# Performance work log

Hardware: AMD Instinct MI355X
Metric: run time of the kernel (lower is better)

## Reference

```python
import jax, jax.numpy as jnp
import numpy as np

HEADS = 8
EPS = 1e-5
CONV_DIMS = [(16, 32), (32, 64), (64, 128), (128, 256), (256, 128), (128, 128)]


def _bn(x, g, b):
    # BatchNorm over the node dimension (training-mode batch statistics)
    m = x.mean(0)
    v = x.var(0)
    return (x - m) * jax.lax.rsqrt(v + EPS) * g + b


def _feast(x, src, dst, W, U, c, bias, n):
    # FeaStConv: q_h = softmax_h(u_h.(x_j - x_i) + c_h); out_i = mean_j sum_h q_h * (W_h x_j) + bias
    q = jax.nn.softmax((x[src] - x[dst]) @ U + c, axis=-1)          # [E, H]
    f = (x[src] @ W).reshape(src.shape[0], HEADS, -1)               # [E, H, C_out]
    msg = jnp.einsum('ehc,eh->ec', f, q)                            # [E, C_out]
    agg = jax.ops.segment_sum(msg, dst, num_segments=n)
    cnt = jax.ops.segment_sum(jnp.ones_like(dst, dtype=msg.dtype), dst, num_segments=n)
    return agg / cnt[:, None] + bias


def reference(pos, x, g0, b0, lin0_W, lin0_b,
              W0, U0, C0, B0, gc0, bc0,
              W1, U1, C1, B1, gc1, bc1,
              W2, U2, C2, B2, gc2, bc2,
              W3, U3, C3, B3, gc3, bc3,
              W4, U4, C4, B4, gc4, bc4,
              W5, U5, C5, B5, gc5, bc5,
              lin1_W, lin1_b, lin2_W, lin2_b, edge_index):
    n = pos.shape[0]
    loops = jnp.arange(n, dtype=edge_index.dtype)                   # PyG FeaStConv adds self-loops
    src = jnp.concatenate([edge_index[0], loops])
    dst = jnp.concatenate([edge_index[1], loops])

    h = _bn(pos, g0, b0)
    h = jnp.concatenate([h, x], axis=1)
    h = jax.nn.relu(h @ lin0_W + lin0_b)

    convs = [(W0, U0, C0, B0, gc0, bc0), (W1, U1, C1, B1, gc1, bc1),
             (W2, U2, C2, B2, gc2, bc2), (W3, U3, C3, B3, gc3, bc3),
             (W4, U4, C4, B4, gc4, bc4), (W5, U5, C5, B5, gc5, bc5)]
    for W, U, c, bias, g, b in convs:
        h = _feast(h, src, dst, W, U, c, bias, n)
        h = jax.nn.relu(_bn(h, g, b))

    h = jax.nn.relu(h @ lin1_W + lin1_b)
    return h @ lin2_W + lin2_b


def setup_inputs() -> dict:
    key = jax.random.key(0)
    N, E = 10000, 160000
    ks = iter(jax.random.split(key, 64))
    d = {}
    d['pos'] = jax.random.normal(next(ks), (N, 2), jnp.float32)
    d['x'] = jax.random.normal(next(ks), (N, 2), jnp.float32)
    d['edge_index'] = jax.random.randint(next(ks), (2, E), 0, N, dtype=jnp.int32)

    def lin(k, i, o):
        return jax.random.normal(k, (i, o), jnp.float32) * np.float32(1.0 / np.sqrt(i))

    d['g0'] = jnp.ones(2, jnp.float32); d['b0'] = jnp.zeros(2, jnp.float32)
    d['lin0_W'] = lin(next(ks), 4, 16); d['lin0_b'] = jnp.zeros(16, jnp.float32)
    for i, (ci, co) in enumerate(CONV_DIMS):
        d[f'W{i}'] = lin(next(ks), ci, HEADS * co)
        d[f'U{i}'] = lin(next(ks), ci, HEADS)
        d[f'C{i}'] = jnp.zeros(HEADS, jnp.float32)
        d[f'B{i}'] = jnp.zeros(co, jnp.float32)
        d[f'gc{i}'] = jnp.ones(co, jnp.float32)
        d[f'bc{i}'] = jnp.zeros(co, jnp.float32)
    d['lin1_W'] = lin(next(ks), 128, 64); d['lin1_b'] = jnp.zeros(64, jnp.float32)
    d['lin2_W'] = lin(next(ks), 64, 2); d['lin2_b'] = jnp.zeros(2, jnp.float32)
    return d
```

## Files before the change

kernel.cpp:

```cpp
#include <hip/hip_runtime.h>
#include <hip/hip_bf16.h>
#include <math.h>

#define HEADS 8
#define EPS 1e-5f

typedef __attribute__((ext_vector_type(8))) _Float16 half8;
typedef __attribute__((ext_vector_type(4))) _Float16 half4;
typedef __attribute__((ext_vector_type(2))) _Float16 half2v;
typedef __attribute__((ext_vector_type(4))) float f32x4;

__device__ __forceinline__ unsigned short f2h(float f) {
    union { _Float16 h; unsigned short u; } v;
    v.h = (_Float16)f;
    return v.u;
}

#define PACK_TOTAL 745472
#define PACK_BLOCKS 2912

__global__ void k_setup1(const float* __restrict__ W0, const float* __restrict__ W1,
                         const float* __restrict__ W2, const float* __restrict__ W3,
                         const float* __restrict__ W4, const float* __restrict__ W5,
                         unsigned short* __restrict__ Bp,
                         const int* __restrict__ ei, int* __restrict__ deg,
                         const float* __restrict__ pos, float* __restrict__ pstats,
                         int E, int N, int degBlocks) {
    int b = blockIdx.x, tid = threadIdx.x;
    if (b < PACK_BLOCKS) {
        int idx = b * 256 + tid;
        const int CI[6]  = {16, 32, 64, 128, 256, 128};
        const int CO[6]  = {32, 64, 128, 256, 128, 128};
        const int COP[6] = {64, 64, 128, 256, 128, 128};
        const int OFF[7] = {0, 8192, 24576, 90112, 352256, 614400, 745472};
        int L = 0;
        while (idx >= OFF[L + 1]) ++L;
        const float* W = L == 0 ? W0 : L == 1 ? W1 : L == 2 ? W2 : L == 3 ? W3 : L == 4 ? W4 : W5;
        int rel = idx - OFF[L];
        int j = rel & 7;
        int lane = (rel >> 3) & 63;
        int t = rel >> 9;
        int nT = COP[L] >> 4;
        int nt = t % nT, kt = t / nT;
        int kk = kt * 32 + ((lane >> 4) << 3) + j;
        int c  = (nt << 4) + (lane & 15);
        int ci = CI[L], co = CO[L];
        float v = 0.f;
        if (c < co) {
            int h = kk / ci, ko = kk % ci;
            v = W[ko * (HEADS * co) + h * co + c];
        }
        Bp[idx] = f2h(v);
    } else if (b < PACK_BLOCKS + degBlocks) {
        int e = (b - PACK_BLOCKS) * 256 + tid;
        int E2 = E + N;
        if (e < E2) {
            int dst = (e < E) ? ei[E + e] : (e - E);
            atomicAdd(&deg[dst], 1);
        }
    } else {
        int gid = (b - PACK_BLOCKS - degBlocks) * 256 + tid;
        int stride = 64 * 256;
        float s0 = 0, s1 = 0, q0 = 0, q1 = 0;
        for (int i = gid; i < N; i += stride) {
            float a = pos[i * 2], bb = pos[i * 2 + 1];
            s0 += a; s1 += bb; q0 += a * a; q1 += bb * bb;
        }
        __shared__ float red[256][4];
        red[tid][0] = s0; red[tid][1] = s1; red[tid][2] = q0; red[tid][3] = q1;
        __syncthreads();
        for (int off = 128; off > 0; off >>= 1) {
            if (tid < off) {
                red[tid][0] += red[tid + off][0]; red[tid][1] += red[tid + off][1];
                red[tid][2] += red[tid + off][2]; red[tid][3] += red[tid + off][3];
            }
            __syncthreads();
        }
        if (tid == 0) {
            atomicAdd(&pstats[0], red[0][0]); atomicAdd(&pstats[1], red[0][1]);
            atomicAdd(&pstats[2], red[0][2]); atomicAdd(&pstats[3], red[0][3]);
        }
    }
}

__global__ void k_scan(const int* __restrict__ deg, int* __restrict__ row_ptr, int n) {
    __shared__ int part[1024];
    int t = threadIdx.x;
    int chunk = (n + 1023) >> 10;
    int begin = t * chunk;
    int end = begin + chunk;
    if (begin > n) begin = n;
    if (end > n) end = n;
    int s = 0;
    for (int i = begin; i < end; ++i) s += deg[i];
    part[t] = s;
    __syncthreads();
    for (int off = 1; off < 1024; off <<= 1) {
        int v = (t >= off) ? part[t - off] : 0;
        __syncthreads();
        part[t] += v;
        __syncthreads();
    }
    int run = (t == 0) ? 0 : part[t - 1];
    for (int i = begin; i < end; ++i) { row_ptr[i] = run; run += deg[i]; }
    if (t == 1023) row_ptr[n] = part[1023];
}

__global__ void k_setup2(const int* __restrict__ ei, const int* __restrict__ row_ptr,
                         int* __restrict__ fill, int* __restrict__ src_sorted,
                         const float* __restrict__ pos, const float* __restrict__ x,
                         const float* __restrict__ pstats, const float* __restrict__ g0,
                         const float* __restrict__ b0, const float* __restrict__ W,
                         const float* __restrict__ bias, const float* __restrict__ U0,
                         _Float16* __restrict__ out, float* __restrict__ xu0,
                         int E, int N, int fillBlocks) {
    int b = blockIdx.x, tid = threadIdx.x;
    if (b < fillBlocks) {
        int e = b * 256 + tid;
        int E2 = E + N;
        if (e < E2) {
            int srcv, dst;
            if (e < E) { srcv = ei[e]; dst = ei[E + e]; } else { srcv = e - E; dst = srcv; }
            int p = atomicAdd(&fill[dst], 1);
            src_sorted[row_ptr[dst] + p] = srcv;
        }
    } else {
        int i = (b - fillBlocks) * 256 + tid;
        if (i >= N) return;
        float invn = 1.0f / (float)N;
        float in4[4];
        #pragma unroll
        for (int j = 0; j < 2; ++j) {
            float m = pstats[j] * invn;
            float v = pstats[2 + j] * invn - m * m;
            in4[j] = (pos[i * 2 + j] - m) * rsqrtf(v + EPS) * g0[j] + b0[j];
        }
        in4[2] = x[i * 2]; in4[3] = x[i * 2 + 1];
        float o16[16];
        #pragma unroll
        for (int o = 0; o < 16; ++o) {
            float s = bias[o];
            #pragma unroll
            for (int j = 0; j < 4; ++j) s += in4[j] * W[j * 16 + o];
            o16[o] = fmaxf(s, 0.f);
            out[i * 16 + o] = (_Float16)o16[o];
        }
        #pragma unroll
        for (int hh = 0; hh < 8; ++hh) {
            float p = 0.f;
            #pragma unroll
            for (int k = 0; k < 16; ++k) p += o16[k] * U0[k * 8 + hh];
            xu0[i * 8 + hh] = p;
        }
    }
}

__device__ __forceinline__ void chunk_softmax(const float* __restrict__ xu,
        const int* __restrict__ srcs, int base, int cnt, int lane,
        float4 xi0, float4 xi1, float4 c0, float4 c1, float dinv,
        float* __restrict__ qrow, int* __restrict__ srow) {
    if (lane < cnt) {
        int s = srcs[base + lane];
        float4 xs0 = *(const float4*)(xu + (size_t)s * 8);
        float4 xs1 = *(const float4*)(xu + (size_t)s * 8 + 4);
        float t[8];
        t[0] = xs0.x - xi0.x + c0.x; t[1] = xs0.y - xi0.y + c0.y;
        t[2] = xs0.z - xi0.z + c0.z; t[3] = xs0.w - xi0.w + c0.w;
        t[4] = xs1.x - xi1.x + c1.x; t[5] = xs1.y - xi1.y + c1.y;
        t[6] = xs1.z - xi1.z + c1.z; t[7] = xs1.w - xi1.w + c1.w;
        float mx = t[0];
        #pragma unroll
        for (int h = 1; h < 8; ++h) mx = fmaxf(mx, t[h]);
        float sum = 0.f;
        #pragma unroll
        for (int h = 0; h < 8; ++h) { t[h] = __expf(t[h] - mx); sum += t[h]; }
        float qs = dinv / sum;
        float4 q0 = {t[0] * qs, t[1] * qs, t[2] * qs, t[3] * qs};
        float4 q1 = {t[4] * qs, t[5] * qs, t[6] * qs, t[7] * qs};
        *(float4*)(qrow + lane * 8) = q0;
        *(float4*)(qrow + lane * 8 + 4) = q1;
        srow[lane] = s;
    }
}

template<int V>
__global__ __launch_bounds__(256) void k_gather_big(const _Float16* __restrict__ zin,
        const float* __restrict__ stats, const float* __restrict__ g,
        const float* __restrict__ b,
        const float* __restrict__ xu, const float* __restrict__ chead,
        const int* __restrict__ row_ptr, const int* __restrict__ srcs,
        unsigned short* __restrict__ S, int n, int ci) {
    __shared__ float qbuf[4][64 * 8];
    __shared__ int   sbuf[4][64];
    int w = threadIdx.x >> 6, lane = threadIdx.x & 63;
    int i = blockIdx.x * 4 + w;
    if (i >= n) return;
    int rp0 = row_ptr[i], rp1 = row_ptr[i + 1];
    float dinv = 1.f / (float)(rp1 - rp0);
    float4 xi0 = *(const float4*)(xu + (size_t)i * 8);
    float4 xi1 = *(const float4*)(xu + (size_t)i * 8 + 4);
    float4 c0 = *(const float4*)chead;
    float4 c1 = *(const float4*)(chead + 4);
    int kb = lane * V;
    float sc[V], bo[V];
    if (stats) {
        float invn = 1.f / (float)n;
        #pragma unroll
        for (int v = 0; v < V; ++v) {
            int c = kb + v;
            float m = stats[c] * invn;
            float var = stats[ci + c] * invn - m * m;
            float s = g[c] * rsqrtf(var + EPS);
            sc[v] = s; bo[v] = b[c] - m * s;
        }
    } else {
        #pragma unroll
        for (int v = 0; v < V; ++v) { sc[v] = 1.f; bo[v] = 0.f; }
    }
    float acc[8][V];
    #pragma unroll
    for (int hh = 0; hh < 8; ++hh)
        #pragma unroll
        for (int v = 0; v < V; ++v) acc[hh][v] = 0.f;

    for (int base = rp0; base < rp1; base += 64) {
        int cnt = rp1 - base; if (cnt > 64) cnt = 64;
        chunk_softmax(xu, srcs, base, cnt, lane, xi0, xi1, c0, c1, dinv, qbuf[w], sbuf[w]);
        for (int j = 0; j < cnt; ++j) {
            int s = sbuf[w][j];
            const _Float16* h0 = zin + (size_t)s * ci + kb;
            float xv[V];
            if (V == 4) {
                half4 f = *(const half4*)h0;
                #pragma unroll
                for (int v = 0; v < 4; ++v) xv[v] = fmaxf((float)f[v] * sc[v] + bo[v], 0.f);
            } else if (V == 2) {
                half2v f = *(const half2v*)h0;
                #pragma unroll
                for (int v = 0; v < 2; ++v) xv[v] = fmaxf((float)f[v] * sc[v] + bo[v], 0.f);
            } else {
                xv[0] = fmaxf((float)h0[0] * sc[0] + bo[0], 0.f);
            }
            const float4* qa = (const float4*)(qbuf[w] + j * 8);
            float4 qa0 = qa[0], qa1 = qa[1];
            float qA[8] = {qa0.x, qa0.y, qa0.z, qa0.w, qa1.x, qa1.y, qa1.z, qa1.w};
            #pragma unroll
            for (int hh = 0; hh < 8; ++hh)
                #pragma unroll
                for (int v = 0; v < V; ++v) acc[hh][v] += qA[hh] * xv[v];
        }
    }
    #pragma unroll
    for (int hh = 0; hh < 8; ++hh) {
        unsigned short o[V];
        #pragma unroll
        for (int v = 0; v < V; ++v) o[v] = f2h(acc[hh][v]);
        unsigned short* sp = S + (size_t)i * 8 * ci + hh * ci + kb;
        if (V == 4)      *(ushort4*)sp = *(ushort4*)o;
        else if (V == 2) *(ushort2*)sp = *(ushort2*)o;
        else             sp[0] = o[0];
    }
}

template<int V2>
__global__ __launch_bounds__(256) void k_gather_small(const _Float16* __restrict__ zin,
        const float* __restrict__ stats, const float* __restrict__ g,
        const float* __restrict__ b,
        const float* __restrict__ xu, const float* __restrict__ chead,
        const int* __restrict__ row_ptr, const int* __restrict__ srcs,
        unsigned short* __restrict__ S, int n) {
    const int ci = 8 * V2;
    __shared__ float qbuf[4][64 * 8];
    __shared__ int   sbuf[4][64];
    int w = threadIdx.x >> 6, lane = threadIdx.x & 63;
    int i = blockIdx.x * 4 + w;
    if (i >= n) return;
    int rp0 = row_ptr[i], rp1 = row_ptr[i + 1];
    float dinv = 1.f / (float)(rp1 - rp0);
    float4 xi0 = *(const float4*)(xu + (size_t)i * 8);
    float4 xi1 = *(const float4*)(xu + (size_t)i * 8 + 4);
    float4 c0 = *(const float4*)chead;
    float4 c1 = *(const float4*)(chead + 4);
    int hh = lane >> 3;
    int kb = (lane & 7) * V2;
    float sc[V2], bo[V2];
    if (stats) {
        float invn = 1.f / (float)n;
        #pragma unroll
        for (int v = 0; v < V2; ++v) {
            int c = kb + v;
            float m = stats[c] * invn;
            float var = stats[ci + c] * invn - m * m;
            float s = g[c] * rsqrtf(var + EPS);
            sc[v] = s; bo[v] = b[c] - m * s;
        }
    } else {
        #pragma unroll
        for (int v = 0; v < V2; ++v) { sc[v] = 1.f; bo[v] = 0.f; }
    }
    float acc[V2];
    #pragma unroll
    for (int v = 0; v < V2; ++v) acc[v] = 0.f;

    for (int base = rp0; base < rp1; base += 64) {
        int cnt = rp1 - base; if (cnt > 64) cnt = 64;
        chunk_softmax(xu, srcs, base, cnt, lane, xi0, xi1, c0, c1, dinv, qbuf[w], sbuf[w]);
        for (int j = 0; j < cnt; ++j) {
            int s = sbuf[w][j];
            const _Float16* h0 = zin + (size_t)s * ci + kb;
            float xv[V2];
            if (V2 == 4) {
                half4 f = *(const half4*)h0;
                #pragma unroll
                for (int v = 0; v < 4; ++v) xv[v] = fmaxf((float)f[v] * sc[v] + bo[v], 0.f);
            } else {
                half2v f = *(const half2v*)h0;
                #pragma unroll
                for (int v = 0; v < 2; ++v) xv[v] = fmaxf((float)f[v] * sc[v] + bo[v], 0.f);
            }
            float q0 = qbuf[w][j * 8 + hh];
            #pragma unroll
            for (int v = 0; v < V2; ++v) acc[v] += q0 * xv[v];
        }
    }
    unsigned short o[V2];
    #pragma unroll
    for (int v = 0; v < V2; ++v) o[v] = f2h(acc[v]);
    unsigned short* sp = S + (size_t)i * 8 * ci + hh * ci + kb;
    if (V2 == 4) *(ushort4*)sp = *(ushort4*)o;
    else         *(ushort2*)sp = *(ushort2*)o;
}

__global__ __launch_bounds__(256) void k_gemm_stats(const unsigned short* __restrict__ A,
        const unsigned short* __restrict__ Bp, _Float16* __restrict__ z,
        float* __restrict__ stats, int M, int K, int co, int nTtot) {
    int tid = threadIdx.x;
    int w = tid >> 6, lane = tid & 63;
    int quad = lane >> 4, l16 = lane & 15;
    int m0 = blockIdx.x * 64;
    int n0 = blockIdx.y * 64;
    int nt0 = n0 >> 4;
    int m = m0 + w * 16 + l16;
    int mc = m < M ? m : M - 1;
    const half8* Ap = (const half8*)(A + (size_t)mc * K) + quad;
    const half8* Bb = (const half8*)Bp;
    f32x4 acc[4] = {};
    int nsteps = K >> 5;
    for (int ks = 0; ks < nsteps; ++ks) {
        half8 a = Ap[ks * 4];
        long bbase = ((long)ks * nTtot + nt0) * 64 + lane;
        #pragma unroll
        for (int ct = 0; ct < 4; ++ct) {
            half8 b = Bb[bbase + ct * 64];
            acc[ct] = __builtin_amdgcn_mfma_f32_16x16x32_f16(a, b, acc[ct], 0, 0, 0);
        }
    }
    __shared__ float sred[64][4];
    __shared__ float qred[64][4];
    #pragma unroll
    for (int ct = 0; ct < 4; ++ct) {
        int colb = ct * 16 + l16;
        int col = n0 + colb;
        float s = 0.f, q = 0.f;
        #pragma unroll
        for (int r = 0; r < 4; ++r) {
            int row = m0 + w * 16 + quad * 4 + r;
            bool ok = row < M;
            float v = ok ? acc[ct][r] : 0.f;
            if (ok && col < co) z[(size_t)row * co + col] = (_Float16)v;
            s += v; q += v * v;
        }
        s += __shfl_xor(s, 16, 64); q += __shfl_xor(q, 16, 64);
        s += __shfl_xor(s, 32, 64); q += __shfl_xor(q, 32, 64);
        if (quad == 0) { sred[colb][w] = s; qred[colb][w] = q; }
    }
    __syncthreads();
    if (tid < 64 && (n0 + tid) < co) {
        float s = sred[tid][0] + sred[tid][1] + sred[tid][2] + sred[tid][3];
        float q = qred[tid][0] + qred[tid][1] + qred[tid][2] + qred[tid][3];
        atomicAdd(&stats[n0 + tid], s);
        atomicAdd(&stats[co + n0 + tid], q);
    }
}

template<int V>
__global__ __launch_bounds__(256) void k_xu(const _Float16* __restrict__ z,
        const float* __restrict__ stats, const float* __restrict__ g,
        const float* __restrict__ b, const float* __restrict__ Un,
        float* __restrict__ xun, int n, int co) {
    int w = threadIdx.x >> 6, lane = threadIdx.x & 63;
    int node = blockIdx.x * 4 + w;
    if (node >= n) return;
    int c0 = lane * V;
    bool act = c0 < co;
    float invn = 1.f / (float)n;
    float p[8];
    #pragma unroll
    for (int hh = 0; hh < 8; ++hh) p[hh] = 0.f;
    if (act) {
        const _Float16* zp = z + (size_t)node * co + c0;
        float hv[V];
        #pragma unroll
        for (int v = 0; v < V; ++v) {
            int c = c0 + v;
            float m = stats[c] * invn;
            float var = stats[co + c] * invn - m * m;
            float s = g[c] * rsqrtf(var + EPS);
            hv[v] = fmaxf((float)zp[v] * s + (b[c] - m * s), 0.f);
        }
        #pragma unroll
        for (int v = 0; v < V; ++v)
            #pragma unroll
            for (int hh = 0; hh < 8; ++hh) p[hh] += hv[v] * Un[(c0 + v) * 8 + hh];
    }
    #pragma unroll
    for (int hh = 0; hh < 8; ++hh) {
        #pragma unroll
        for (int off = 32; off; off >>= 1) p[hh] += __shfl_xor(p[hh], off, 64);
    }
    float mine = 0.f;
    #pragma unroll
    for (int hh = 0; hh < 8; ++hh) if (lane == hh) mine = p[hh];
    if (lane < 8) xun[node * 8 + lane] = mine;
}

__global__ __launch_bounds__(256) void k_bnlin(const _Float16* __restrict__ z,
        const float* __restrict__ stats, const float* __restrict__ g,
        const float* __restrict__ b, const float* __restrict__ W1,
        const float* __restrict__ b1, const float* __restrict__ W2,
        const float* __restrict__ b2, float* __restrict__ out, int n) {
    __shared__ float hbuf[4][128];
    int w = threadIdx.x >> 6, lane = threadIdx.x & 63;
    int node = blockIdx.x * 4 + w;
    if (node >= n) return;
    float invn = 1.f / (float)n;
    half2v zv = *(const half2v*)(z + (size_t)node * 128 + lane * 2);
    #pragma unroll
    for (int v = 0; v < 2; ++v) {
        int c = lane * 2 + v;
        float mm = stats[c] * invn;
        float vr = stats[128 + c] * invn - mm * mm;
        float s = g[c] * rsqrtf(vr + EPS);
        hbuf[w][c] = fmaxf((float)zv[v] * s + (b[c] - mm * s), 0.f);
    }
    float s = b1[lane];
    #pragma unroll 8
    for (int k = 0; k < 128; ++k) s += hbuf[w][k] * W1[k * 64 + lane];
    float r = fmaxf(s, 0.f);
    float p0 = r * W2[lane * 2];
    float p1 = r * W2[lane * 2 + 1];
    #pragma unroll
    for (int off = 32; off > 0; off >>= 1) {
        p0 += __shfl_down(p0, off, 64);
        p1 += __shfl_down(p1, off, 64);
    }
    if (lane == 0) {
        out[node * 2] = p0 + b2[0];
        out[node * 2 + 1] = p1 + b2[1];
    }
}

extern "C" void kernel_launch(void* const* d_in, const int* in_sizes, int n_in,
                              void* d_out, int out_size, void* d_ws, size_t ws_size,
                              hipStream_t stream) {
    const float* pos    = (const float*)d_in[0];
    const float* x      = (const float*)d_in[1];
    const int*   ei     = (const int*)d_in[2];
    const float* g0     = (const float*)d_in[3];
    const float* b0     = (const float*)d_in[4];
    const float* lin0_W = (const float*)d_in[5];
    const float* lin0_b = (const float*)d_in[6];
    const float* lin1_W = (const float*)d_in[43];
    const float* lin1_b = (const float*)d_in[44];
    const float* lin2_W = (const float*)d_in[45];
    const float* lin2_b = (const float*)d_in[46];

    int N = in_sizes[0] / 2;
    int E = in_sizes[2] / 2;
    int E2 = E + N;

    static const int CI[6]  = {16, 32, 64, 128, 256, 128};
    static const int CO[6]  = {32, 64, 128, 256, 128, 128};
    static const int COP[6] = {64, 64, 128, 256, 128, 128};
    static const int BPOFF[6] = {0, 8192, 24576, 90112, 352256, 614400};

    char* p = (char*)d_ws;
    auto alloc = [&](size_t bytes) -> char* {
        char* r = p;
        p += (bytes + 255) & ~(size_t)255;
        return r;
    };
    unsigned short* BpAll = (unsigned short*)alloc((size_t)PACK_TOTAL * 2);
    char* zr = alloc(((size_t)2 * N + 4 + 6 * 512) * 4);
    int*   deg      = (int*)zr;
    int*   fill     = deg + N;
    float* pstats   = (float*)(fill + N);
    float* statsAll = pstats + 4;
    size_t zr_bytes = ((size_t)2 * N + 4 + 6 * 512) * 4;

    int* row_ptr    = (int*)alloc(((size_t)N + 1) * 4);
    int* src_sorted = (int*)alloc((size_t)E2 * 4);
    float* xu       = (float*)alloc((size_t)N * 8 * 4);
    unsigned short* S = (unsigned short*)alloc((size_t)N * 2048 * 2);
    _Float16* z     = (_Float16*)alloc((size_t)N * 256 * 2);
    _Float16* hA    = (_Float16*)alloc((size_t)N * 16 * 2);

    hipMemsetAsync(zr, 0, zr_bytes, stream);

    const int tpb = 256;
    int degBlocks = (E2 + tpb - 1) / tpb;
    int fillBlocks = degBlocks;
    int frontBlocks = (N + tpb - 1) / tpb;

    k_setup1<<<PACK_BLOCKS + degBlocks + 64, tpb, 0, stream>>>(
        (const float*)d_in[7], (const float*)d_in[13], (const float*)d_in[19],
        (const float*)d_in[25], (const float*)d_in[31], (const float*)d_in[37], BpAll,
        ei, deg, pos, pstats, E, N, degBlocks);
    k_scan<<<1, 1024, 0, stream>>>(deg, row_ptr, N);
    k_setup2<<<fillBlocks + frontBlocks, tpb, 0, stream>>>(
        ei, row_ptr, fill, src_sorted, pos, x, pstats, g0, b0, lin0_W, lin0_b,
        (const float*)d_in[8], hA, xu, E, N, fillBlocks);

    for (int L = 0; L < 6; ++L) {
        int ci = CI[L], co = CO[L], coP = COP[L];
        const float* Ch = (const float*)d_in[7 + L * 6 + 2];
        const float* gc = (const float*)d_in[7 + L * 6 + 4];
        const float* bc = (const float*)d_in[7 + L * 6 + 5];
        const float* Un = (L < 5) ? (const float*)d_in[7 + (L + 1) * 6 + 1] : nullptr;
        int K = HEADS * ci;
        float* statsL = statsAll + L * 512;

        const _Float16* zin = (L == 0) ? hA : z;
        const float* pstatsL = (L == 0) ? nullptr : statsAll + (L - 1) * 512;
        const float* gPrev   = (L == 0) ? nullptr : (const float*)d_in[7 + (L - 1) * 6 + 4];
        const float* bPrev   = (L == 0) ? nullptr : (const float*)d_in[7 + (L - 1) * 6 + 5];

        int ggrid = (N + 3) / 4;
        if (ci == 16)       k_gather_small<2><<<ggrid, 256, 0, stream>>>(zin, pstatsL, gPrev, bPrev, xu, Ch, row_ptr, src_sorted, S, N);
        else if (ci == 32)  k_gather_small<4><<<ggrid, 256, 0, stream>>>(zin, pstatsL, gPrev, bPrev, xu, Ch, row_ptr, src_sorted, S, N);
        else if (ci == 64)  k_gather_big<1><<<ggrid, 256, 0, stream>>>(zin, pstatsL, gPrev, bPrev, xu, Ch, row_ptr, src_sorted, S, N, ci);
        else if (ci == 128) k_gather_big<2><<<ggrid, 256, 0, stream>>>(zin, pstatsL, gPrev, bPrev, xu, Ch, row_ptr, src_sorted, S, N, ci);
        else                k_gather_big<4><<<ggrid, 256, 0, stream>>>(zin, pstatsL, gPrev, bPrev, xu, Ch, row_ptr, src_sorted, S, N, ci);

        dim3 g((N + 63) / 64, coP / 64);
        k_gemm_stats<<<g, 256, 0, stream>>>(S, BpAll + BPOFF[L], z, statsL, N, K, co, coP / 16);

        int bgrid = (N + 3) / 4;
        if (L < 5) {
            if (co >= 256)      k_xu<4><<<bgrid, 256, 0, stream>>>(z, statsL, gc, bc, Un, xu, N, co);
            else if (co >= 128) k_xu<2><<<bgrid, 256, 0, stream>>>(z, statsL, gc, bc, Un, xu, N, co);
            else                k_xu<1><<<bgrid, 256, 0, stream>>>(z, statsL, gc, bc, Un, xu, N, co);
        } else {
            k_bnlin<<<bgrid, 256, 0, stream>>>(z, statsL, gc, bc, lin1_W, lin1_b, lin2_W, lin2_b,
                                               (float*)d_out, N);
        }
    }
}
```

Baseline: 441.9 us.

## Fuse gather-aggregate with MFMA GEMM and stats for wide FeaSt layers

For layers with ci >= 64, the per-node weighted gather now writes its head-scaled aggregates into a shared-memory A tile of 16 nodes. The same block then runs the MFMA GEMM against the packed weights, writes z, and atomically accumulates the BN statistics, so the large S intermediate is no longer written to and read back from global memory. z is ping-ponged between two buffers because the fused kernel reads the previous layer's z while writing the new one. In exchange, each wave now processes 4 nodes serially, and the large LDS tile (about 66KB at ci=256) may reduce occupancy.

New measurement: 607.1 us. +37.4%, slower.

```diff
diff --git a/kernel.cpp b/kernel.cpp
--- a/kernel.cpp
+++ b/kernel.cpp
@@ -184,81 +184,132 @@
 }
 
 template<int V>
-__global__ __launch_bounds__(256) void k_gather_big(const _Float16* __restrict__ zin,
-        const float* __restrict__ stats, const float* __restrict__ g,
+__global__ __launch_bounds__(256) void k_fused(const _Float16* __restrict__ zin,
+        const float* __restrict__ pstats, const float* __restrict__ g,
         const float* __restrict__ b,
         const float* __restrict__ xu, const float* __restrict__ chead,
         const int* __restrict__ row_ptr, const int* __restrict__ srcs,
-        unsigned short* __restrict__ S, int n, int ci) {
+        const unsigned short* __restrict__ Bp, _Float16* __restrict__ z,
+        float* __restrict__ statsOut, int n, int nT) {
+    const int ci = 64 * V;
+    const int K  = 8 * ci;
+    const int SH = K + 8;
+    const int NSTEP = K / 32;
+    __shared__ _Float16 A[16 * SH];
     __shared__ float qbuf[4][64 * 8];
     __shared__ int   sbuf[4][64];
     int w = threadIdx.x >> 6, lane = threadIdx.x & 63;
-    int i = blockIdx.x * 4 + w;
-    if (i >= n) return;
-    int rp0 = row_ptr[i], rp1 = row_ptr[i + 1];
-    float dinv = 1.f / (float)(rp1 - rp0);
-    float4 xi0 = *(const float4*)(xu + (size_t)i * 8);
-    float4 xi1 = *(const float4*)(xu + (size_t)i * 8 + 4);
+    int quad = lane >> 4, l16 = lane & 15;
+    int base = blockIdx.x * 16;
+
+    int kb = lane * V;
+    float sc[V], bo[V];
+    if (pstats) {
+        float invn = 1.f / (float)n;
+        #pragma unroll
+        for (int v = 0; v < V; ++v) {
+            int c = kb + v;
+            float m = pstats[c] * invn;
+            float var = pstats[ci + c] * invn - m * m;
+            float s = g[c] * rsqrtf(var + EPS);
+            sc[v] = s; bo[v] = b[c] - m * s;
+        }
+    } else {
+        #pragma unroll
+        for (int v = 0; v < V; ++v) { sc[v] = 1.f; bo[v] = 0.f; }
+    }
     float4 c0 = *(const float4*)chead;
     float4 c1 = *(const float4*)(chead + 4);
-    int kb = lane * V;
-    float sc[V], bo[V];
-    if (stats) {
-        float invn = 1.f / (float)n;
-        #pragma unroll
-        for (int v = 0; v < V; ++v) {
-            int c = kb + v;
-            float m = stats[c] * invn;
-            float var = stats[ci + c] * invn - m * m;
-            float s = g[c] * rsqrtf(var + EPS);
-            sc[v] = s; bo[v] = b[c] - m * s;
-        }
-    } else {
-        #pragma unroll
-        for (int v = 0; v < V; ++v) { sc[v] = 1.f; bo[v] = 0.f; }
-    }
-    float acc[8][V];
-    #pragma unroll
-    for (int hh = 0; hh < 8; ++hh)
-        #pragma unroll
-        for (int v = 0; v < V; ++v) acc[hh][v] = 0.f;
-
-    for (int base = rp0; base < rp1; base += 64) {
-        int cnt = rp1 - base; if (cnt > 64) cnt = 64;
-        chunk_softmax(xu, srcs, base, cnt, lane, xi0, xi1, c0, c1, dinv, qbuf[w], sbuf[w]);
-        for (int j = 0; j < cnt; ++j) {
-            int s = sbuf[w][j];
-            const _Float16* h0 = zin + (size_t)s * ci + kb;
-            float xv[V];
-            if (V == 4) {
-                half4 f = *(const half4*)h0;
+
+    for (int t = 0; t < 4; ++t) {
+        int i = base + w * 4 + t;
+        int ic = i < n ? i : n - 1;
+        int rp0 = row_ptr[ic], rp1 = row_ptr[ic + 1];
+        float dinv = 1.f / (float)(rp1 - rp0);
+        float4 xi0 = *(const float4*)(xu + (size_t)ic * 8);
+        float4 xi1 = *(const float4*)(xu + (size_t)ic * 8 + 4);
+        float acc[8][V];
+        #pragma unroll
+        for (int hh = 0; hh < 8; ++hh)
+            #pragma unroll
+            for (int v = 0; v < V; ++v) acc[hh][v] = 0.f;
+        for (int bse = rp0; bse < rp1; bse += 64) {
+            int cnt = rp1 - bse; if (cnt > 64) cnt = 64;
+            chunk_softmax(xu, srcs, bse, cnt, lane, xi0, xi1, c0, c1, dinv, qbuf[w], sbuf[w]);
+            for (int j = 0; j < cnt; ++j) {
+                int s = sbuf[w][j];
+                const _Float16* h0 = zin + (size_t)s * ci + kb;
+                float xv[V];
+                if (V == 4) {
+                    half4 f = *(const half4*)h0;
+                    #pragma unroll
+                    for (int v = 0; v < 4; ++v) xv[v] = fmaxf((float)f[v] * sc[v] + bo[v], 0.f);
+                } else if (V == 2) {
+                    half2v f = *(const half2v*)h0;
+                    #pragma unroll
+                    for (int v = 0; v < 2; ++v) xv[v] = fmaxf((float)f[v] * sc[v] + bo[v], 0.f);
+                } else {
+                    xv[0] = fmaxf((float)h0[0] * sc[0] + bo[0], 0.f);
+                }
+                const float4* qa = (const float4*)(qbuf[w] + j * 8);
+                float4 qa0 = qa[0], qa1 = qa[1];
+                float qA[8] = {qa0.x, qa0.y, qa0.z, qa0.w, qa1.x, qa1.y, qa1.z, qa1.w};
                 #pragma unroll
-                for (int v = 0; v < 4; ++v) xv[v] = fmaxf((float)f[v] * sc[v] + bo[v], 0.f);
-            } else if (V == 2) {
-                half2v f = *(const half2v*)h0;
-                #pragma unroll
-                for (int v = 0; v < 2; ++v) xv[v] = fmaxf((float)f[v] * sc[v] + bo[v], 0.f);
-            } else {
-                xv[0] = fmaxf((float)h0[0] * sc[0] + bo[0], 0.f);
+                for (int hh = 0; hh < 8; ++hh)
+                    #pragma unroll
+                    for (int v = 0; v < V; ++v) acc[hh][v] += qA[hh] * xv[v];
             }
-            const float4* qa = (const float4*)(qbuf[w] + j * 8);
-            float4 qa0 = qa[0], qa1 = qa[1];
-            float qA[8] = {qa0.x, qa0.y, qa0.z, qa0.w, qa1.x, qa1.y, qa1.z, qa1.w};
+        }
+        int m = w * 4 + t;
+        #pragma unroll
+        for (int hh = 0; hh < 8; ++hh) {
+            _Float16 o[V];
             #pragma unroll
-            for (int hh = 0; hh < 8; ++hh)
-                #pragma unroll
-                for (int v = 0; v < V; ++v) acc[hh][v] += qA[hh] * xv[v];
-        }
-    }
-    #pragma unroll
-    for (int hh = 0; hh < 8; ++hh) {
-        unsigned short o[V];
-        #pragma unroll
-        for (int v = 0; v < V; ++v) o[v] = f2h(acc[hh][v]);
-        unsigned short* sp = S + (size_t)i * 8 * ci + hh * ci + kb;
-        if (V == 4)      *(ushort4*)sp = *(ushort4*)o;
-        else if (V == 2) *(ushort2*)sp = *(ushort2*)o;
-        else             sp[0] = o[0];
+            for (int v = 0; v < V; ++v) o[v] = (_Float16)acc[hh][v];
+            _Float16* ap = &A[m * SH + hh * ci + kb];
+            if (V == 4)      *(half4*)ap = *(half4*)o;
+            else if (V == 2) *(half2v*)ap = *(half2v*)o;
+            else             ap[0] = o[0];
+        }
+    }
+    __syncthreads();
+
+    int TT = nT >> 2;
+    const half8* Bb = (const half8*)Bp;
+    f32x4 acc[4] = {};
+    for (int ks = 0; ks < NSTEP; ++ks) {
+        half8 a = *(const half8*)&A[l16 * SH + ks * 32 + quad * 8];
+        #pragma unroll
+        for (int tt = 0; tt < 4; ++tt) {
+            if (tt < TT) {
+                int nt = w + (tt << 2);
+                half8 bfr = Bb[((long)ks * nT + nt) * 64 + lane];
+                acc[tt] = __builtin_amdgcn_mfma_f32_16x16x32_f16(a, bfr, acc[tt], 0, 0, 0);
+            }
+        }
+    }
+    int co = nT * 16;
+    #pragma unroll
+    for (int tt = 0; tt < 4; ++tt) {
+        if (tt < TT) {
+            int nt = w + (tt << 2);
+            int col = nt * 16 + l16;
+            float s = 0.f, q = 0.f;
+            #pragma unroll
+            for (int r = 0; r < 4; ++r) {
+                int node = base + quad * 4 + r;
+                bool ok = node < n;
+                float v = ok ? acc[tt][r] : 0.f;
+                if (ok) z[(size_t)node * co + col] = (_Float16)v;
+                s += v; q += v * v;
+            }
+            s += __shfl_xor(s, 16, 64); q += __shfl_xor(q, 16, 64);
+            s += __shfl_xor(s, 32, 64); q += __shfl_xor(q, 32, 64);
+            if (quad == 0) {
+                atomicAdd(&statsOut[col], s);
+                atomicAdd(&statsOut[co + col], q);
+            }
+        }
     }
 }
 
@@ -501,8 +552,9 @@
     int* row_ptr    = (int*)alloc(((size_t)N + 1) * 4);
     int* src_sorted = (int*)alloc((size_t)E2 * 4);
     float* xu       = (float*)alloc((size_t)N * 8 * 4);
-    unsigned short* S = (unsigned short*)alloc((size_t)N * 2048 * 2);
-    _Float16* z     = (_Float16*)alloc((size_t)N * 256 * 2);
+    unsigned short* S = (unsigned short*)alloc((size_t)N * 8 * 32 * 2);
+    _Float16* zA    = (_Float16*)alloc((size_t)N * 256 * 2);
+    _Float16* zB    = (_Float16*)alloc((size_t)N * 256 * 2);
     _Float16* hA    = (_Float16*)alloc((size_t)N * 16 * 2);
 
     hipMemsetAsync(zr, 0, zr_bytes, stream);
@@ -521,6 +573,8 @@
         ei, row_ptr, fill, src_sorted, pos, x, pstats, g0, b0, lin0_W, lin0_b,
         (const float*)d_in[8], hA, xu, E, N, fillBlocks);
 
+    const _Float16* zin = hA;
+    _Float16* zout = zA;
     for (int L = 0; L < 6; ++L) {
         int ci = CI[L], co = CO[L], coP = COP[L];
         const float* Ch = (const float*)d_in[7 + L * 6 + 2];
@@ -530,29 +584,40 @@
         int K = HEADS * ci;
         float* statsL = statsAll + L * 512;
 
-        const _Float16* zin = (L == 0) ? hA : z;
         const float* pstatsL = (L == 0) ? nullptr : statsAll + (L - 1) * 512;
         const float* gPrev   = (L == 0) ? nullptr : (const float*)d_in[7 + (L - 1) * 6 + 4];
         const float* bPrev   = (L == 0) ? nullptr : (const float*)d_in[7 + (L - 1) * 6 + 5];
 
-        int ggrid = (N + 3) / 4;
-        if (ci == 16)       k_gather_small<2><<<ggrid, 256, 0, stream>>>(zin, pstatsL, gPrev, bPrev, xu, Ch, row_ptr, src_sorted, S, N);
-        else if (ci == 32)  k_gather_small<4><<<ggrid, 256, 0, stream>>>(zin, pstatsL, gPrev, bPrev, xu, Ch, row_ptr, src_sorted, S, N);
-        else if (ci == 64)  k_gather_big<1><<<ggrid, 256, 0, stream>>>(zin, pstatsL, gPrev, bPrev, xu, Ch, row_ptr, src_sorted, S, N, ci);
-        else if (ci == 128) k_gather_big<2><<<ggrid, 256, 0, stream>>>(zin, pstatsL, gPrev, bPrev, xu, Ch, row_ptr, src_sorted, S, N, ci);
-        else                k_gather_big<4><<<ggrid, 256, 0, stream>>>(zin, pstatsL, gPrev, bPrev, xu, Ch, row_ptr, src_sorted, S, N, ci);
-
-        dim3 g((N + 63) / 64, coP / 64);
-        k_gemm_stats<<<g, 256, 0, stream>>>(S, BpAll + BPOFF[L], z, statsL, N, K, co, coP / 16);
+        if (ci < 64) {
+            int ggrid = (N + 3) / 4;
+            if (ci == 16) k_gather_small<2><<<ggrid, 256, 0, stream>>>(zin, pstatsL, gPrev, bPrev, xu, Ch, row_ptr, src_sorted, S, N);
+            else          k_gather_small<4><<<ggrid, 256, 0, stream>>>(zin, pstatsL, gPrev, bPrev, xu, Ch, row_ptr, src_sorted, S, N);
+            dim3 g((N + 63) / 64, coP / 64);
+            k_gemm_stats<<<g, 256, 0, stream>>>(S, BpAll + BPOFF[L], zout, statsL, N, K, co, coP / 16);
+        } else {
+            int fgrid = (N + 15) / 16;
+            if (ci == 64)
+                k_fused<1><<<fgrid, 256, 0, stream>>>(zin, pstatsL, gPrev, bPrev, xu, Ch, row_ptr, src_sorted,
+                                                      BpAll + BPOFF[L], zout, statsL, N, coP / 16);
+            else if (ci == 128)
+                k_fused<2><<<fgrid, 256, 0, stream>>>(zin, pstatsL, gPrev, bPrev, xu, Ch, row_ptr, src_sorted,
+                                                      BpAll + BPOFF[L], zout, statsL, N, coP / 16);
+            else
+                k_fused<4><<<fgrid, 256, 0, stream>>>(zin, pstatsL, gPrev, bPrev, xu, Ch, row_ptr, src_sorted,
+                                                      BpAll + BPOFF[L], zout, statsL, N, coP / 16);
+        }
 
         int bgrid = (N + 3) / 4;
         if (L < 5) {
-            if (co >= 256)      k_xu<4><<<bgrid, 256, 0, stream>>>(z, statsL, gc, bc, Un, xu, N, co);
-            else if (co >= 128) k_xu<2><<<bgrid, 256, 0, stream>>>(z, statsL, gc, bc, Un, xu, N, co);
-            else                k_xu<1><<<bgrid, 256, 0, stream>>>(z, statsL, gc, bc, Un, xu, N, co);
+            if (co >= 256)      k_xu<4><<<bgrid, 256, 0, stream>>>(zout, statsL, gc, bc, Un, xu, N, co);
+            else if (co >= 128) k_xu<2><<<bgrid, 256, 0, stream>>>(zout, statsL, gc, bc, Un, xu, N, co);
+            else                k_xu<1><<<bgrid, 256, 0, stream>>>(zout, statsL, gc, bc, Un, xu, N, co);
         } else {
-            k_bnlin<<<bgrid, 256, 0, stream>>>(z, statsL, gc, bc, lin1_W, lin1_b, lin2_W, lin2_b,
+            k_bnlin<<<bgrid, 256, 0, stream>>>(zout, statsL, gc, bc, lin1_W, lin1_b, lin2_W, lin2_b,
                                                (float*)d_out, N);
         }
-    }
-}
+
+        zin = zout;
+        zout = (zout == zA) ? zB : zA;
+    }
+}
```
